# Performance work log

Measured on AMD Instinct MI355X. Metric: run time of the kernel, lower is better.

## Reference

```python
import jax, jax.numpy as jnp
import numpy as np
import math

H = 2048      # hidden_size
NH = 32       # num heads
HD = H // NH  # head_dim = 64
THETA = 10000.0
B, S = 2, 2048


def _rope_tables(seq_len):
    inv_freq = 1.0 / (THETA ** (jnp.arange(0, HD, 2, dtype=jnp.float32) / HD))
    t = jnp.arange(seq_len, dtype=jnp.float32)
    freqs = t[:, None] * inv_freq[None, :]          # [S, HD/2]
    emb = jnp.concatenate([freqs, freqs], axis=-1)  # [S, HD]
    return jnp.cos(emb)[None, None], jnp.sin(emb)[None, None]  # [1,1,S,HD]


def _rotate_half(x):
    x1, x2 = jnp.split(x, 2, axis=-1)
    return jnp.concatenate([-x2, x1], axis=-1)


def setup_inputs() -> dict:
    key = jax.random.key(0)
    ks = jax.random.split(key, 5)
    hidden_states = jax.random.normal(ks[0], (B, S, H), dtype=jnp.float32)
    wscale = 1.0 / math.sqrt(H)
    wq = jax.random.normal(ks[1], (H, H), dtype=jnp.float32) * wscale
    wk = jax.random.normal(ks[2], (H, H), dtype=jnp.float32) * wscale
    wv = jax.random.normal(ks[3], (H, H), dtype=jnp.float32) * wscale
    wo = jax.random.normal(ks[4], (H, H), dtype=jnp.float32) * wscale
    # additive causal mask: 0 on/below diagonal, -1e9 above
    causal = jnp.tril(jnp.ones((S, S), dtype=bool))
    attention_mask = jnp.where(causal, 0.0, -1e9).astype(jnp.float32)[None, None]
    return {"hidden_states": hidden_states, "attention_mask": attention_mask,
            "wq": wq, "wk": wk, "wv": wv, "wo": wo}


def reference(hidden_states, attention_mask, wq, wk, wv, wo):
    b, s, _ = hidden_states.shape
    # projections (Linear, no bias); weights stored [in, out]
    q = (hidden_states @ wq).reshape(b, s, NH, HD).transpose(0, 2, 1, 3)  # [B,NH,S,HD]
    k = (hidden_states @ wk).reshape(b, s, NH, HD).transpose(0, 2, 1, 3)
    v = (hidden_states @ wv).reshape(b, s, NH, HD).transpose(0, 2, 1, 3)
    # RoPE
    cos, sin = _rope_tables(s)
    q = q * cos + _rotate_half(q) * sin
    k = k * cos + _rotate_half(k) * sin
    # attention
    attn = jnp.einsum('bhqd,bhkd->bhqk', q, k) / math.sqrt(HD)
    attn = attn + attention_mask
    w = jax.nn.softmax(attn, axis=-1)
    out = jnp.einsum('bhqk,bhkd->bhqd', w, v)           # [B,NH,S,HD]
    out = out.transpose(0, 2, 1, 3).reshape(b, s, H)    # [B,S,H]
    return out @ wo
```

## Files before the change

kernel.cpp:

```cpp
#include <hip/hip_runtime.h>
#include <hip/hip_bf16.h>

#define H 2048
#define NH 32
#define HD 64
#define BB 2
#define SS 2048
#define MM (BB*SS)

typedef __attribute__((ext_vector_type(8))) short bf16x8;
typedef __attribute__((ext_vector_type(4))) float f32x4;
typedef __attribute__((ext_vector_type(16))) float f32x16;
typedef unsigned short u16;
typedef unsigned int u32;
typedef __attribute__((ext_vector_type(4))) u32 u32x4;

static __device__ __forceinline__ u16 f2bf(float f){
  union { float f; u32 i; } v; v.f = f;
  u32 x = v.i;
  return (u16)((x + 0x7FFFu + ((x >> 16) & 1u)) >> 16);
}
static __device__ __forceinline__ float bf2f(u16 u){
  union { u32 i; float f; } v; v.i = ((u32)u) << 16; return v.f;
}
static __device__ __forceinline__ u32 pk2(float a, float b){
  u32 r;
  asm("v_cvt_pk_bf16_f32 %0, %1, %2" : "=v"(r) : "v"(a), "v"(b));
  return r;
}

static __device__ __forceinline__ void gload16(const u16* g, u16* l){
  __builtin_amdgcn_global_load_lds((const __attribute__((address_space(1))) void*)g,
                                   (__attribute__((address_space(3))) void*)l, 16, 0, 0);
}

__global__ void k_cvt(const float* __restrict__ src, u16* __restrict__ dst){
  const int i = (blockIdx.x * 256 + threadIdx.x) * 4;
  float4 v = *(const float4*)(src + i);
  ushort4 o;
  o.x = f2bf(v.x); o.y = f2bf(v.y); o.z = f2bf(v.z); o.w = f2bf(v.w);
  *(ushort4*)(dst + i) = o;
}

__global__ void k_wtrans(const float* __restrict__ w0, const float* __restrict__ w1,
                         const float* __restrict__ w2, const float* __restrict__ w3,
                         u16* __restrict__ d0, u16* __restrict__ d1,
                         u16* __restrict__ d2, u16* __restrict__ d3){
  __shared__ float tile[32][33];
  const int z = blockIdx.z;
  const float* w = z==0 ? w0 : z==1 ? w1 : z==2 ? w2 : w3;
  u16* d        = z==0 ? d0 : z==1 ? d1 : z==2 ? d2 : d3;
  const int n0 = blockIdx.x * 32, k0 = blockIdx.y * 32;
  const int tx = threadIdx.x, ty = threadIdx.y;
  #pragma unroll
  for (int j = 0; j < 4; j++)
    tile[ty + 8*j][tx] = w[(size_t)(k0 + ty + 8*j) * H + n0 + tx];
  __syncthreads();
  #pragma unroll
  for (int j = 0; j < 4; j++)
    d[(size_t)(n0 + ty + 8*j) * H + k0 + tx] = f2bf(tile[tx][ty + 8*j]);
}

__global__ __launch_bounds__(512, 2) void k_gemm8(
    const u16* __restrict__ A, const u16* __restrict__ Bt,
    u16* __restrict__ CQ, u16* __restrict__ CK, u16* __restrict__ CV,
    int M, int K){
  __shared__ __align__(16) u16 As[2][128][64];
  __shared__ __align__(16) u16 Bs[2][384][64];
  const int flat = blockIdx.x;
  const int id = (flat & 7) * 64 + (flat >> 3);
  const int gy = id >> 5, gx = id & 31;
  const int m0 = gx * 128, n0 = gy * 384;
  const int t = threadIdx.x, w = t >> 6, l = t & 63;
  const int wm = w >> 2, wn = w & 3;
  const int lrow = l & 15, lk = (l >> 4) * 8;
  const int sw = (lrow & 7) * 8;
  const int sr = t >> 3, sc = (t & 7) * 8;
  const int ssc = sc ^ ((sr & 7) * 8);
  const int NK = K >> 6;

  auto stageA = [&](int kt, int u){
    const size_t kb = (size_t)kt * 64 + ssc;
    #pragma unroll
    for (int c = 0; c < 2; c++)
      gload16(A + (size_t)(m0 + c*64 + sr) * K + kb, &As[u][c*64 + sr][sc]);
  };
  auto stageB = [&](int kt, int u){
    const size_t kb = (size_t)kt * 64 + ssc;
    #pragma unroll
    for (int c = 0; c < 6; c++)
      gload16(Bt + (size_t)(n0 + c*64 + sr) * K + kb, &Bs[u][c*64 + sr][sc]);
  };

  f32x4 acc[4][6] = {};

  stageA(0, 0); stageB(0, 0);
  stageA(1, 1); stageB(1, 1);
  asm volatile("s_waitcnt vmcnt(8)" ::: "memory");
  __builtin_amdgcn_s_barrier();

  #pragma unroll 1
  for (int kt = 0; kt < NK; ++kt){
    const int u = kt & 1;
    const bool more = (kt + 2 < NK);
    bf16x8 b0[6], b1[6], a0, a1;

    #pragma unroll
    for (int n = 0; n < 6; n++)
      b0[n] = *(const bf16x8*)&Bs[u][wn*96 + n*16 + lrow][lk ^ sw];
    a0 = *(const bf16x8*)&As[u][wm*64 +  0 + lrow][lk ^ sw];
    a1 = *(const bf16x8*)&As[u][wm*64 + 16 + lrow][lk ^ sw];
    __builtin_amdgcn_s_setprio(1);
    #pragma unroll
    for (int n = 0; n < 6; n++){
      acc[0][n] = __builtin_amdgcn_mfma_f32_16x16x32_bf16(a0, b0[n], acc[0][n], 0, 0, 0);
      acc[1][n] = __builtin_amdgcn_mfma_f32_16x16x32_bf16(a1, b0[n], acc[1][n], 0, 0, 0);
    }
    __builtin_amdgcn_s_setprio(0);
    __builtin_amdgcn_s_barrier();

    #pragma unroll
    for (int n = 0; n < 6; n++)
      b1[n] = *(const bf16x8*)&Bs[u][wn*96 + n*16 + lrow][(32 + lk) ^ sw];
    a0 = *(const bf16x8*)&As[u][wm*64 +  0 + lrow][(32 + lk) ^ sw];
    a1 = *(const bf16x8*)&As[u][wm*64 + 16 + lrow][(32 + lk) ^ sw];
    __builtin_amdgcn_s_setprio(1);
    #pragma unroll
    for (int n = 0; n < 6; n++){
      acc[0][n] = __builtin_amdgcn_mfma_f32_16x16x32_bf16(a0, b1[n], acc[0][n], 0, 0, 0);
      acc[1][n] = __builtin_amdgcn_mfma_f32_16x16x32_bf16(a1, b1[n], acc[1][n], 0, 0, 0);
    }
    __builtin_amdgcn_s_setprio(0);
    __builtin_amdgcn_s_barrier();

    if (more) stageB(kt + 2, u);
    a0 = *(const bf16x8*)&As[u][wm*64 + 32 + lrow][lk ^ sw];
    a1 = *(const bf16x8*)&As[u][wm*64 + 48 + lrow][lk ^ sw];
    __builtin_amdgcn_s_setprio(1);
    #pragma unroll
    for (int n = 0; n < 6; n++){
      acc[2][n] = __builtin_amdgcn_mfma_f32_16x16x32_bf16(a0, b0[n], acc[2][n], 0, 0, 0);
      acc[3][n] = __builtin_amdgcn_mfma_f32_16x16x32_bf16(a1, b0[n], acc[3][n], 0, 0, 0);
    }
    __builtin_amdgcn_s_setprio(0);
    __builtin_amdgcn_s_barrier();

    a0 = *(const bf16x8*)&As[u][wm*64 + 32 + lrow][(32 + lk) ^ sw];
    a1 = *(const bf16x8*)&As[u][wm*64 + 48 + lrow][(32 + lk) ^ sw];
    __builtin_amdgcn_s_setprio(1);
    #pragma unroll
    for (int n = 0; n < 6; n++){
      acc[2][n] = __builtin_amdgcn_mfma_f32_16x16x32_bf16(a0, b1[n], acc[2][n], 0, 0, 0);
      acc[3][n] = __builtin_amdgcn_mfma_f32_16x16x32_bf16(a1, b1[n], acc[3][n], 0, 0, 0);
    }
    __builtin_amdgcn_s_setprio(0);
    __builtin_amdgcn_s_barrier();

    if (more){
      stageA(kt + 2, u);
      asm volatile("s_waitcnt vmcnt(8)" ::: "memory");
      __builtin_amdgcn_s_barrier();
    } else if (kt + 1 < NK){
      asm volatile("s_waitcnt vmcnt(0)" ::: "memory");
      __builtin_amdgcn_s_barrier();
    }
  }

  #pragma unroll
  for (int m = 0; m < 4; m++)
    #pragma unroll
    for (int n = 0; n < 6; n++){
      const int ncol = n0 + wn*96 + n*16 + lrow;
      const int z = ncol >> 11;
      u16* C = (z == 0 ? CQ : z == 1 ? CK : CV) + (ncol & 2047);
      #pragma unroll
      for (int r = 0; r < 4; r++){
        const int row = m0 + wm*64 + m*16 + (l >> 4)*4 + r;
        C[(size_t)row * H] = f2bf(acc[m][n][r]);
      }
    }
}

template<typename OutT>
__global__ __launch_bounds__(256, 2) void k_gemm(
    const u16* __restrict__ A,
    const u16* __restrict__ B0, const u16* __restrict__ B1, const u16* __restrict__ B2,
    OutT* __restrict__ C0, OutT* __restrict__ C1, OutT* __restrict__ C2,
    int M, int N, int K){
  __shared__ __align__(16) u16 As[128][64];
  __shared__ __align__(16) u16 Bs[128][64];
  const int z = blockIdx.z;
  const u16* Bt = z==0 ? B0 : z==1 ? B1 : B2;
  OutT* C       = z==0 ? C0 : z==1 ? C1 : C2;
  const int t = threadIdx.x;
  const int w = t >> 6, l = t & 63;
  const int m0 = blockIdx.x * 128, n0 = blockIdx.y * 128;
  const int srow = t >> 3, scol = (t & 7) * 8;
  const int lrow = l & 15, lk = (l >> 4) * 8;
  const int wr = (w >> 1) * 64, wc = (w & 1) * 64;
  f32x4 acc[4][4] = {};
  for (int k0 = 0; k0 < K; k0 += 64){
    __syncthreads();
    #pragma unroll
    for (int c = 0; c < 4; c++)
      gload16(A + (size_t)(m0 + c*32 + srow) * K + k0 + scol, &As[c*32 + srow][scol]);
    #pragma unroll
    for (int c = 0; c < 4; c++)
      gload16(Bt + (size_t)(n0 + c*32 + srow) * K + k0 + scol, &Bs[c*32 + srow][scol]);
    __syncthreads();
    #pragma unroll
    for (int kk = 0; kk < 2; kk++){
      bf16x8 a[4], b[4];
      #pragma unroll
      for (int m = 0; m < 4; m++) a[m] = *(const bf16x8*)&As[wr + m*16 + lrow][kk*32 + lk];
      #pragma unroll
      for (int n = 0; n < 4; n++) b[n] = *(const bf16x8*)&Bs[wc + n*16 + lrow][kk*32 + lk];
      #pragma unroll
      for (int m = 0; m < 4; m++)
        #pragma unroll
        for (int n = 0; n < 4; n++)
          acc[m][n] = __builtin_amdgcn_mfma_f32_16x16x32_bf16(a[m], b[n], acc[m][n], 0, 0, 0);
    }
  }
  #pragma unroll
  for (int m = 0; m < 4; m++)
    #pragma unroll
    for (int n = 0; n < 4; n++)
      #pragma unroll
      for (int r = 0; r < 4; r++){
        const int row = m0 + wr + m*16 + (l >> 4)*4 + r;
        const int col = n0 + wc + n*16 + lrow;
        const float v = acc[m][n][r];
        if constexpr (sizeof(OutT) == 2) C[(size_t)row * N + col] = (OutT)f2bf(v);
        else                             C[(size_t)row * N + col] = v;
      }
}

__global__ void k_rope(u16* __restrict__ Q, u16* __restrict__ Kp){
  const int idx = blockIdx.x * 256 + threadIdx.x;
  const int quad = idx & 3;
  const int h = (idx >> 2) & 31;
  const int row = idx >> 7;
  const int s = row & (SS - 1);
  const int i0 = quad * 8;
  u16* q = Q  + (size_t)row * H + h * HD;
  u16* k = Kp + (size_t)row * H + h * HD;
  uint4 q1v = *(const uint4*)(q + i0);
  uint4 q2v = *(const uint4*)(q + i0 + 32);
  uint4 k1v = *(const uint4*)(k + i0);
  uint4 k2v = *(const uint4*)(k + i0 + 32);
  u16* q1 = (u16*)&q1v; u16* q2 = (u16*)&q2v;
  u16* k1 = (u16*)&k1v; u16* k2 = (u16*)&k2v;
  const float sf = (float)s;
  const float QSC = 0.18033688011112042f;
  #pragma unroll
  for (int e = 0; e < 8; e++){
    const int i = i0 + e;
    const float inv = exp2f(-0.4152410118609203f * (float)i);
    float rev = sf * inv * 0.15915494309189535f;
    rev -= floorf(rev);
    const float sn = __builtin_amdgcn_sinf(rev);
    const float cs = __builtin_amdgcn_cosf(rev);
    const float qa = bf2f(q1[e]), qb = bf2f(q2[e]);
    q1[e] = f2bf((qa*cs - qb*sn) * QSC);
    q2[e] = f2bf((qb*cs + qa*sn) * QSC);
    const float ka = bf2f(k1[e]), kb = bf2f(k2[e]);
    k1[e] = f2bf(ka*cs - kb*sn);
    k2[e] = f2bf(kb*cs + ka*sn);
  }
  *(uint4*)(q + i0)      = q1v;
  *(uint4*)(q + i0 + 32) = q2v;
  *(uint4*)(k + i0)      = k1v;
  *(uint4*)(k + i0 + 32) = k2v;
}

__global__ __launch_bounds__(256, 2) void k_attn(
    const u16* __restrict__ Q, const u16* __restrict__ K,
    const u16* __restrict__ V, u16* __restrict__ O){
  __shared__ __align__(16) u16 Ks[3][64][64];
  __shared__ __align__(16) u16 Vs[2][64][72];
  const int t = threadIdx.x, w = t >> 6, l = t & 63;
  const int x = blockIdx.x, bh = blockIdx.y;
  const int b = bh >> 5, h = bh & 31;
  const u16* kp = K + (size_t)(b*SS) * H + h * HD;
  const u16* vp = V + (size_t)(b*SS) * H + h * HD;
  const int sr = t >> 3, sc = (t & 7) * 8;
  const int ssc = sc ^ ((sr & 7) * 8);
  const int hi = l >> 5, lq = l & 31;

  auto stageK = [&](int tile, int buf){
    const int jb = tile * 64;
    gload16(kp + (size_t)(jb + sr) * H + ssc,      &Ks[buf][sr][sc]);
    gload16(kp + (size_t)(jb + 32 + sr) * H + ssc, &Ks[buf][32 + sr][sc]);
  };
  auto loadV = [&](int tile, uint4* vv){
    const int jb = tile * 64;
    vv[0] = *(const uint4*)(vp + (size_t)(jb + sr) * H + sc);
    vv[1] = *(const uint4*)(vp + (size_t)(jb + 32 + sr) * H + sc);
  };
  auto publishV = [&](const uint4* vv, int buf){
    #pragma unroll
    for (int c = 0; c < 2; c++){
      const int j = c*32 + sr;
      const u16* pv = (const u16*)&vv[c];
      #pragma unroll
      for (int e = 0; e < 8; e++){
        const int d = sc + e;
        Vs[buf][d][j ^ ((d >> 3) * 8)] = pv[e];
      }
    }
  };

  #pragma unroll 1
  for (int pp = 0; pp < 2; pp++){
    const int qt = pp ? x : (15 - x);
    const int NT = 2*qt + 2;
    const int qw0 = qt*128 + w*32;
    const int qrow = qw0 + lq;

    const u16* qptr = Q + (size_t)(b*SS + qrow) * H + h * HD + hi*8;
    bf16x8 qf[4];
    #pragma unroll
    for (int c = 0; c < 4; c++) qf[c] = *(const bf16x8*)(qptr + c*16);

    float mrun = -1e30f, lrun = 0.f;
    f32x16 oacc[2] = {};
    uint4 vvE[2], vvO[2];

    stageK(0, 0); loadV(0, vvE);
    stageK(1, 1); loadV(1, vvO);
    asm volatile("s_waitcnt vmcnt(4)" ::: "memory");
    publishV(vvE, 0);
    asm volatile("s_waitcnt lgkmcnt(0)" ::: "memory");
    __builtin_amdgcn_s_barrier();

    auto body = [&](int jt, int p, uint4* vvSelf, const uint4* vvOther){
      const int j0 = jt * 64;
      if (jt + 2 < NT){ stageK(jt + 2, (jt + 2) % 3); loadV(jt + 2, vvSelf); }

      if (j0 <= qw0){
        const int kbuf = jt % 3;
        f32x16 sv[2] = {};
        __builtin_amdgcn_s_setprio(1);
        #pragma unroll
        for (int kb = 0; kb < 2; kb++){
          const int row = kb*32 + lq;
          #pragma unroll
          for (int c = 0; c < 4; c++){
            bf16x8 kf = *(const bf16x8*)&Ks[kbuf][row][(c*16 + hi*8) ^ ((row & 7) * 8)];
            sv[kb] = __builtin_amdgcn_mfma_f32_32x32x16_bf16(kf, qf[c], sv[kb], 0, 0, 0);
          }
        }
        __builtin_amdgcn_s_setprio(0);
        if (j0 + 63 > qw0){
          #pragma unroll
          for (int kb = 0; kb < 2; kb++)
            #pragma unroll
            for (int r = 0; r < 16; r++){
              const int kg = j0 + kb*32 + (r & 3) + 8*(r >> 2) + 4*hi;
              if (kg > qrow) sv[kb][r] = -1e30f;
            }
        }
        float t16[16], t8[8], t4[4];
        #pragma unroll
        for (int r = 0; r < 16; r++) t16[r] = fmaxf(sv[0][r], sv[1][r]);
        #pragma unroll
        for (int r = 0; r < 8; r++) t8[r] = fmaxf(t16[r], t16[r+8]);
        #pragma unroll
        for (int r = 0; r < 4; r++) t4[r] = fmaxf(t8[r], t8[r+4]);
        float tm = fmaxf(fmaxf(t4[0], t4[2]), fmaxf(t4[1], t4[3]));
        tm = fmaxf(tm, __shfl_xor(tm, 32, 64));
        if (__any(tm > mrun)){
          const float mn = fmaxf(mrun, tm);
          const float fac = exp2f(mrun - mn);
          mrun = mn;
          lrun *= fac;
          #pragma unroll
          for (int db = 0; db < 2; db++)
            #pragma unroll
            for (int r = 0; r < 16; r++) oacc[db][r] *= fac;
        }
        #pragma unroll
        for (int kb = 0; kb < 2; kb++)
          #pragma unroll
          for (int r = 0; r < 16; r++) sv[kb][r] = exp2f(sv[kb][r] - mrun);
        float s16[16], s8[8], s4[4];
        #pragma unroll
        for (int r = 0; r < 16; r++) s16[r] = sv[0][r] + sv[1][r];
        #pragma unroll
        for (int r = 0; r < 8; r++) s8[r] = s16[r] + s16[r+8];
        #pragma unroll
        for (int r = 0; r < 4; r++) s4[r] = s8[r] + s8[r+4];
        float rs = (s4[0] + s4[1]) + (s4[2] + s4[3]);
        rs += __shfl_xor(rs, 32, 64);
        lrun += rs;
        u32x4 pw[4];
        #pragma unroll
        for (int kb = 0; kb < 2; kb++){
          #pragma unroll
          for (int half = 0; half < 2; half++){
            const int rb = half * 8;
            const u32 own0 = pk2(sv[kb][rb+0], sv[kb][rb+1]);
            const u32 own1 = pk2(sv[kb][rb+2], sv[kb][rb+3]);
            const u32 own2 = pk2(sv[kb][rb+4], sv[kb][rb+5]);
            const u32 own3 = pk2(sv[kb][rb+6], sv[kb][rb+7]);
            const u32 s0 = hi ? own0 : own2;
            const u32 s1 = hi ? own1 : own3;
            const u32 r0 = __shfl_xor(s0, 32, 64);
            const u32 r1 = __shfl_xor(s1, 32, 64);
            u32x4 pv;
            pv[0] = hi ? r0 : own0;
            pv[1] = hi ? r1 : own1;
            pv[2] = hi ? own2 : r0;
            pv[3] = hi ? own3 : r1;
            pw[kb*2 + half] = pv;
          }
        }
        __builtin_amdgcn_s_setprio(1);
        #pragma unroll
        for (int db = 0; db < 2; db++){
          const int d = db*32 + lq;
          #pragma unroll
          for (int tt = 0; tt < 4; tt++){
            bf16x8 vf = *(const bf16x8*)&Vs[p][d][(tt*16 + hi*8) ^ ((d >> 3) * 8)];
            bf16x8 pfr = __builtin_bit_cast(bf16x8, pw[tt]);
            oacc[db] = __builtin_amdgcn_mfma_f32_32x32x16_bf16(vf, pfr, oacc[db], 0, 0, 0);
          }
        }
        __builtin_amdgcn_s_setprio(0);
      }

      if (jt + 2 < NT) asm volatile("s_waitcnt vmcnt(4)" ::: "memory");
      else             asm volatile("s_waitcnt vmcnt(0)" ::: "memory");
      if (jt + 1 < NT) publishV(vvOther, p ^ 1);
      asm volatile("s_waitcnt lgkmcnt(0)" ::: "memory");
      __builtin_amdgcn_s_barrier();
    };

    #pragma unroll 1
    for (int jt2 = 0; jt2 < NT; jt2 += 2){
      body(jt2,     0, vvE, vvO);
      body(jt2 + 1, 1, vvO, vvE);
    }

    const float rl = 1.0f / lrun;
    u16* op = O + (size_t)(b*SS + qrow) * H + h * HD;
    #pragma unroll
    for (int db = 0; db < 2; db++)
      #pragma unroll
      for (int rq = 0; rq < 4; rq++){
        ushort4 o4;
        o4.x = f2bf(oacc[db][rq*4 + 0] * rl);
        o4.y = f2bf(oacc[db][rq*4 + 1] * rl);
        o4.z = f2bf(oacc[db][rq*4 + 2] * rl);
        o4.w = f2bf(oacc[db][rq*4 + 3] * rl);
        *(ushort4*)(op + db*32 + rq*8 + 4*hi) = o4;
      }
  }
}

extern "C" void kernel_launch(void* const* d_in, const int* in_sizes, int n_in,
                              void* d_out, int out_size, void* d_ws, size_t ws_size,
                              hipStream_t stream){
  (void)in_sizes; (void)n_in; (void)out_size; (void)ws_size;
  const float* hs = (const float*)d_in[0];
  const float* wq = (const float*)d_in[2];
  const float* wk = (const float*)d_in[3];
  const float* wv = (const float*)d_in[4];
  const float* wo = (const float*)d_in[5];
  float* out = (float*)d_out;
  char* ws = (char*)d_ws;

  u16* Xb  = (u16*)ws;
  u16* Wqt = (u16*)(ws + (size_t)MM * H * 2);
  u16* Wkt = Wqt + (size_t)H * H;
  u16* Wvt = Wkt + (size_t)H * H;
  u16* Wot = Wvt + (size_t)H * H;
  u16* Vb  = Wot + (size_t)H * H;
  u16* Ob  = Vb  + (size_t)MM * H;
  u16* Qb  = (u16*)d_out;
  u16* Kb  = Qb + (size_t)MM * H;

  k_cvt<<<8192, 256, 0, stream>>>(hs, Xb);
  k_wtrans<<<dim3(64, 64, 4), dim3(32, 8), 0, stream>>>(wq, wk, wv, wo, Wqt, Wkt, Wvt, Wot);
  k_gemm8<<<512, 512, 0, stream>>>(Xb, Wqt, Qb, Kb, Vb, MM, H);
  k_rope<<<2048, 256, 0, stream>>>(Qb, Kb);
  k_attn<<<dim3(8, 64), 256, 0, stream>>>(Qb, Kb, Vb, Ob);
  k_gemm<float><<<dim3(32, 16, 1), 256, 0, stream>>>(Ob, Wot, Wot, Wot, out, out, out, MM, H, H);
}
```

Before: 296.0 us.

## Restructure QKV GEMM inner loop into four phases with explicit LDS wait scheduling

After: 319.1 us. +7.8%, slower.

```diff
diff --git a/kernel.cpp b/kernel.cpp
--- a/kernel.cpp
+++ b/kernel.cpp
@@ -103,61 +103,77 @@
   for (int kt = 0; kt < NK; ++kt){
     const int u = kt & 1;
     const bool more = (kt + 2 < NK);
-    bf16x8 b0[6], b1[6], a0, a1;
-
-    #pragma unroll
-    for (int n = 0; n < 6; n++)
-      b0[n] = *(const bf16x8*)&Bs[u][wn*96 + n*16 + lrow][lk ^ sw];
-    a0 = *(const bf16x8*)&As[u][wm*64 +  0 + lrow][lk ^ sw];
-    a1 = *(const bf16x8*)&As[u][wm*64 + 16 + lrow][lk ^ sw];
+    bf16x8 a[4], b[3];
+
+    #pragma unroll
+    for (int mb = 0; mb < 4; mb++)
+      a[mb] = *(const bf16x8*)&As[u][wm*64 + mb*16 + lrow][lk ^ sw];
+    #pragma unroll
+    for (int nb = 0; nb < 3; nb++)
+      b[nb] = *(const bf16x8*)&Bs[u][wn*96 + nb*16 + lrow][lk ^ sw];
+    __builtin_amdgcn_sched_barrier(0);
+    __builtin_amdgcn_s_barrier();
+    asm volatile("s_waitcnt lgkmcnt(0)" ::: "memory");
     __builtin_amdgcn_s_setprio(1);
     #pragma unroll
-    for (int n = 0; n < 6; n++){
-      acc[0][n] = __builtin_amdgcn_mfma_f32_16x16x32_bf16(a0, b0[n], acc[0][n], 0, 0, 0);
-      acc[1][n] = __builtin_amdgcn_mfma_f32_16x16x32_bf16(a1, b0[n], acc[1][n], 0, 0, 0);
-    }
+    for (int mb = 0; mb < 4; mb++)
+      #pragma unroll
+      for (int nb = 0; nb < 3; nb++)
+        acc[mb][nb] = __builtin_amdgcn_mfma_f32_16x16x32_bf16(a[mb], b[nb], acc[mb][nb], 0, 0, 0);
     __builtin_amdgcn_s_setprio(0);
     __builtin_amdgcn_s_barrier();
 
     #pragma unroll
-    for (int n = 0; n < 6; n++)
-      b1[n] = *(const bf16x8*)&Bs[u][wn*96 + n*16 + lrow][(32 + lk) ^ sw];
-    a0 = *(const bf16x8*)&As[u][wm*64 +  0 + lrow][(32 + lk) ^ sw];
-    a1 = *(const bf16x8*)&As[u][wm*64 + 16 + lrow][(32 + lk) ^ sw];
+    for (int nb = 0; nb < 3; nb++)
+      b[nb] = *(const bf16x8*)&Bs[u][wn*96 + 48 + nb*16 + lrow][lk ^ sw];
+    __builtin_amdgcn_sched_barrier(0);
+    __builtin_amdgcn_s_barrier();
+    asm volatile("s_waitcnt lgkmcnt(0)" ::: "memory");
     __builtin_amdgcn_s_setprio(1);
     #pragma unroll
-    for (int n = 0; n < 6; n++){
-      acc[0][n] = __builtin_amdgcn_mfma_f32_16x16x32_bf16(a0, b1[n], acc[0][n], 0, 0, 0);
-      acc[1][n] = __builtin_amdgcn_mfma_f32_16x16x32_bf16(a1, b1[n], acc[1][n], 0, 0, 0);
-    }
+    for (int mb = 0; mb < 4; mb++)
+      #pragma unroll
+      for (int nb = 0; nb < 3; nb++)
+        acc[mb][3 + nb] = __builtin_amdgcn_mfma_f32_16x16x32_bf16(a[mb], b[nb], acc[mb][3 + nb], 0, 0, 0);
     __builtin_amdgcn_s_setprio(0);
     __builtin_amdgcn_s_barrier();
 
-    if (more) stageB(kt + 2, u);
-    a0 = *(const bf16x8*)&As[u][wm*64 + 32 + lrow][lk ^ sw];
-    a1 = *(const bf16x8*)&As[u][wm*64 + 48 + lrow][lk ^ sw];
+    #pragma unroll
+    for (int mb = 0; mb < 4; mb++)
+      a[mb] = *(const bf16x8*)&As[u][wm*64 + mb*16 + lrow][(32 + lk) ^ sw];
+    #pragma unroll
+    for (int nb = 0; nb < 3; nb++)
+      b[nb] = *(const bf16x8*)&Bs[u][wn*96 + nb*16 + lrow][(32 + lk) ^ sw];
+    __builtin_amdgcn_sched_barrier(0);
+    __builtin_amdgcn_s_barrier();
+    asm volatile("s_waitcnt lgkmcnt(0)" ::: "memory");
     __builtin_amdgcn_s_setprio(1);
     #pragma unroll
-    for (int n = 0; n < 6; n++){
-      acc[2][n] = __builtin_amdgcn_mfma_f32_16x16x32_bf16(a0, b0[n], acc[2][n], 0, 0, 0);
-      acc[3][n] = __builtin_amdgcn_mfma_f32_16x16x32_bf16(a1, b0[n], acc[3][n], 0, 0, 0);
-    }
+    for (int mb = 0; mb < 4; mb++)
+      #pragma unroll
+      for (int nb = 0; nb < 3; nb++)
+        acc[mb][nb] = __builtin_amdgcn_mfma_f32_16x16x32_bf16(a[mb], b[nb], acc[mb][nb], 0, 0, 0);
     __builtin_amdgcn_s_setprio(0);
     __builtin_amdgcn_s_barrier();
 
-    a0 = *(const bf16x8*)&As[u][wm*64 + 32 + lrow][(32 + lk) ^ sw];
-    a1 = *(const bf16x8*)&As[u][wm*64 + 48 + lrow][(32 + lk) ^ sw];
+    #pragma unroll
+    for (int nb = 0; nb < 3; nb++)
+      b[nb] = *(const bf16x8*)&Bs[u][wn*96 + 48 + nb*16 + lrow][(32 + lk) ^ sw];
+    if (more) stageA(kt + 2, u);
+    __builtin_amdgcn_sched_barrier(0);
+    __builtin_amdgcn_s_barrier();
+    asm volatile("s_waitcnt lgkmcnt(0)" ::: "memory");
     __builtin_amdgcn_s_setprio(1);
     #pragma unroll
-    for (int n = 0; n < 6; n++){
-      acc[2][n] = __builtin_amdgcn_mfma_f32_16x16x32_bf16(a0, b1[n], acc[2][n], 0, 0, 0);
-      acc[3][n] = __builtin_amdgcn_mfma_f32_16x16x32_bf16(a1, b1[n], acc[3][n], 0, 0, 0);
-    }
+    for (int mb = 0; mb < 4; mb++)
+      #pragma unroll
+      for (int nb = 0; nb < 3; nb++)
+        acc[mb][3 + nb] = __builtin_amdgcn_mfma_f32_16x16x32_bf16(a[mb], b[nb], acc[mb][3 + nb], 0, 0, 0);
     __builtin_amdgcn_s_setprio(0);
     __builtin_amdgcn_s_barrier();
 
     if (more){
-      stageA(kt + 2, u);
+      stageB(kt + 2, u);
       asm volatile("s_waitcnt vmcnt(8)" ::: "memory");
       __builtin_amdgcn_s_barrier();
     } else if (kt + 1 < NK){
```

## Pipeline output projection GEMM with double-buffered LDS and fuse Q RoPE into attention

Applied to the files above, without the earlier changes.

After: 287.8 us. 2.8% less time.

```diff
diff --git a/kernel.cpp b/kernel.cpp
--- a/kernel.cpp
+++ b/kernel.cpp
@@ -181,78 +181,135 @@
     }
 }
 
-template<typename OutT>
-__global__ __launch_bounds__(256, 2) void k_gemm(
-    const u16* __restrict__ A,
-    const u16* __restrict__ B0, const u16* __restrict__ B1, const u16* __restrict__ B2,
-    OutT* __restrict__ C0, OutT* __restrict__ C1, OutT* __restrict__ C2,
-    int M, int N, int K){
-  __shared__ __align__(16) u16 As[128][64];
-  __shared__ __align__(16) u16 Bs[128][64];
-  const int z = blockIdx.z;
-  const u16* Bt = z==0 ? B0 : z==1 ? B1 : B2;
-  OutT* C       = z==0 ? C0 : z==1 ? C1 : C2;
-  const int t = threadIdx.x;
-  const int w = t >> 6, l = t & 63;
-  const int m0 = blockIdx.x * 128, n0 = blockIdx.y * 128;
-  const int srow = t >> 3, scol = (t & 7) * 8;
+__global__ __launch_bounds__(512, 2) void k_gemmo(
+    const u16* __restrict__ A, const u16* __restrict__ Bt,
+    float* __restrict__ C, int M, int N, int K){
+  __shared__ __align__(16) u16 As[2][128][64];
+  __shared__ __align__(16) u16 Bs[2][256][64];
+  const int flat = blockIdx.x;
+  const int id = (flat & 7) * 32 + (flat >> 3);
+  const int gy = id >> 5, gx = id & 31;
+  const int m0 = gx * 128, n0 = gy * 256;
+  const int t = threadIdx.x, w = t >> 6, l = t & 63;
+  const int wm = w >> 2, wn = w & 3;
   const int lrow = l & 15, lk = (l >> 4) * 8;
-  const int wr = (w >> 1) * 64, wc = (w & 1) * 64;
+  const int sw = (lrow & 7) * 8;
+  const int sr = t >> 3, sc = (t & 7) * 8;
+  const int ssc = sc ^ ((sr & 7) * 8);
+  const int NK = K >> 6;
+
+  auto stageA = [&](int kt, int u){
+    const size_t kb = (size_t)kt * 64 + ssc;
+    #pragma unroll
+    for (int c = 0; c < 2; c++)
+      gload16(A + (size_t)(m0 + c*64 + sr) * K + kb, &As[u][c*64 + sr][sc]);
+  };
+  auto stageB = [&](int kt, int u){
+    const size_t kb = (size_t)kt * 64 + ssc;
+    #pragma unroll
+    for (int c = 0; c < 4; c++)
+      gload16(Bt + (size_t)(n0 + c*64 + sr) * K + kb, &Bs[u][c*64 + sr][sc]);
+  };
+
   f32x4 acc[4][4] = {};
-  for (int k0 = 0; k0 < K; k0 += 64){
-    __syncthreads();
-    #pragma unroll
-    for (int c = 0; c < 4; c++)
-      gload16(A + (size_t)(m0 + c*32 + srow) * K + k0 + scol, &As[c*32 + srow][scol]);
-    #pragma unroll
-    for (int c = 0; c < 4; c++)
-      gload16(Bt + (size_t)(n0 + c*32 + srow) * K + k0 + scol, &Bs[c*32 + srow][scol]);
-    __syncthreads();
-    #pragma unroll
-    for (int kk = 0; kk < 2; kk++){
-      bf16x8 a[4], b[4];
-      #pragma unroll
-      for (int m = 0; m < 4; m++) a[m] = *(const bf16x8*)&As[wr + m*16 + lrow][kk*32 + lk];
-      #pragma unroll
-      for (int n = 0; n < 4; n++) b[n] = *(const bf16x8*)&Bs[wc + n*16 + lrow][kk*32 + lk];
-      #pragma unroll
-      for (int m = 0; m < 4; m++)
-        #pragma unroll
-        for (int n = 0; n < 4; n++)
-          acc[m][n] = __builtin_amdgcn_mfma_f32_16x16x32_bf16(a[m], b[n], acc[m][n], 0, 0, 0);
+
+  stageA(0, 0); stageB(0, 0);
+  stageA(1, 1); stageB(1, 1);
+  asm volatile("s_waitcnt vmcnt(6)" ::: "memory");
+  __builtin_amdgcn_s_barrier();
+
+  #pragma unroll 1
+  for (int kt = 0; kt < NK; ++kt){
+    const int u = kt & 1;
+    const bool more = (kt + 2 < NK);
+    bf16x8 b0[4], b1[4], a0, a1;
+
+    #pragma unroll
+    for (int n = 0; n < 4; n++)
+      b0[n] = *(const bf16x8*)&Bs[u][wn*64 + n*16 + lrow][lk ^ sw];
+    a0 = *(const bf16x8*)&As[u][wm*64 +  0 + lrow][lk ^ sw];
+    a1 = *(const bf16x8*)&As[u][wm*64 + 16 + lrow][lk ^ sw];
+    __builtin_amdgcn_s_setprio(1);
+    #pragma unroll
+    for (int n = 0; n < 4; n++){
+      acc[0][n] = __builtin_amdgcn_mfma_f32_16x16x32_bf16(a0, b0[n], acc[0][n], 0, 0, 0);
+      acc[1][n] = __builtin_amdgcn_mfma_f32_16x16x32_bf16(a1, b0[n], acc[1][n], 0, 0, 0);
+    }
+    __builtin_amdgcn_s_setprio(0);
+    __builtin_amdgcn_s_barrier();
+
+    #pragma unroll
+    for (int n = 0; n < 4; n++)
+      b1[n] = *(const bf16x8*)&Bs[u][wn*64 + n*16 + lrow][(32 + lk) ^ sw];
+    a0 = *(const bf16x8*)&As[u][wm*64 +  0 + lrow][(32 + lk) ^ sw];
+    a1 = *(const bf16x8*)&As[u][wm*64 + 16 + lrow][(32 + lk) ^ sw];
+    __builtin_amdgcn_s_setprio(1);
+    #pragma unroll
+    for (int n = 0; n < 4; n++){
+      acc[0][n] = __builtin_amdgcn_mfma_f32_16x16x32_bf16(a0, b1[n], acc[0][n], 0, 0, 0);
+      acc[1][n] = __builtin_amdgcn_mfma_f32_16x16x32_bf16(a1, b1[n], acc[1][n], 0, 0, 0);
+    }
+    __builtin_amdgcn_s_setprio(0);
+    __builtin_amdgcn_s_barrier();
+
+    if (more) stageB(kt + 2, u);
+    a0 = *(const bf16x8*)&As[u][wm*64 + 32 + lrow][lk ^ sw];
+    a1 = *(const bf16x8*)&As[u][wm*64 + 48 + lrow][lk ^ sw];
+    __builtin_amdgcn_s_setprio(1);
+    #pragma unroll
+    for (int n = 0; n < 4; n++){
+      acc[2][n] = __builtin_amdgcn_mfma_f32_16x16x32_bf16(a0, b0[n], acc[2][n], 0, 0, 0);
+      acc[3][n] = __builtin_amdgcn_mfma_f32_16x16x32_bf16(a1, b0[n], acc[3][n], 0, 0, 0);
+    }
+    __builtin_amdgcn_s_setprio(0);
+    __builtin_amdgcn_s_barrier();
+
+    a0 = *(const bf16x8*)&As[u][wm*64 + 32 + lrow][(32 + lk) ^ sw];
+    a1 = *(const bf16x8*)&As[u][wm*64 + 48 + lrow][(32 + lk) ^ sw];
+    __builtin_amdgcn_s_setprio(1);
+    #pragma unroll
+    for (int n = 0; n < 4; n++){
+      acc[2][n] = __builtin_amdgcn_mfma_f32_16x16x32_bf16(a0, b1[n], acc[2][n], 0, 0, 0);
+      acc[3][n] = __builtin_amdgcn_mfma_f32_16x16x32_bf16(a1, b1[n], acc[3][n], 0, 0, 0);
+    }
+    __builtin_amdgcn_s_setprio(0);
+    __builtin_amdgcn_s_barrier();
+
+    if (more){
+      stageA(kt + 2, u);
+      asm volatile("s_waitcnt vmcnt(6)" ::: "memory");
+      __builtin_amdgcn_s_barrier();
+    } else if (kt + 1 < NK){
+      asm volatile("s_waitcnt vmcnt(0)" ::: "memory");
+      __builtin_amdgcn_s_barrier();
     }
   }
+
   #pragma unroll
   for (int m = 0; m < 4; m++)
     #pragma unroll
-    for (int n = 0; n < 4; n++)
+    for (int n = 0; n < 4; n++){
+      const int col = n0 + wn*64 + n*16 + lrow;
       #pragma unroll
       for (int r = 0; r < 4; r++){
-        const int row = m0 + wr + m*16 + (l >> 4)*4 + r;
-        const int col = n0 + wc + n*16 + lrow;
-        const float v = acc[m][n][r];
-        if constexpr (sizeof(OutT) == 2) C[(size_t)row * N + col] = (OutT)f2bf(v);
-        else                             C[(size_t)row * N + col] = v;
+        const int row = m0 + wm*64 + m*16 + (l >> 4)*4 + r;
+        C[(size_t)row * N + col] = acc[m][n][r];
       }
-}
-
-__global__ void k_rope(u16* __restrict__ Q, u16* __restrict__ Kp){
+    }
+}
+
+__global__ void k_rope(u16* __restrict__ Kp){
   const int idx = blockIdx.x * 256 + threadIdx.x;
   const int quad = idx & 3;
   const int h = (idx >> 2) & 31;
   const int row = idx >> 7;
   const int s = row & (SS - 1);
   const int i0 = quad * 8;
-  u16* q = Q  + (size_t)row * H + h * HD;
   u16* k = Kp + (size_t)row * H + h * HD;
-  uint4 q1v = *(const uint4*)(q + i0);
-  uint4 q2v = *(const uint4*)(q + i0 + 32);
   uint4 k1v = *(const uint4*)(k + i0);
   uint4 k2v = *(const uint4*)(k + i0 + 32);
-  u16* q1 = (u16*)&q1v; u16* q2 = (u16*)&q2v;
   u16* k1 = (u16*)&k1v; u16* k2 = (u16*)&k2v;
   const float sf = (float)s;
-  const float QSC = 0.18033688011112042f;
   #pragma unroll
   for (int e = 0; e < 8; e++){
     const int i = i0 + e;
@@ -261,15 +318,10 @@
     rev -= floorf(rev);
     const float sn = __builtin_amdgcn_sinf(rev);
     const float cs = __builtin_amdgcn_cosf(rev);
-    const float qa = bf2f(q1[e]), qb = bf2f(q2[e]);
-    q1[e] = f2bf((qa*cs - qb*sn) * QSC);
-    q2[e] = f2bf((qb*cs + qa*sn) * QSC);
     const float ka = bf2f(k1[e]), kb = bf2f(k2[e]);
     k1[e] = f2bf(ka*cs - kb*sn);
     k2[e] = f2bf(kb*cs + ka*sn);
   }
-  *(uint4*)(q + i0)      = q1v;
-  *(uint4*)(q + i0 + 32) = q2v;
   *(uint4*)(k + i0)      = k1v;
   *(uint4*)(k + i0 + 32) = k2v;
 }
@@ -287,6 +339,7 @@
   const int sr = t >> 3, sc = (t & 7) * 8;
   const int ssc = sc ^ ((sr & 7) * 8);
   const int hi = l >> 5, lq = l & 31;
+  const float QSC = 0.18033688011112042f;
 
   auto stageK = [&](int tile, int buf){
     const int jb = tile * 64;
@@ -319,9 +372,32 @@
     const int qrow = qw0 + lq;
 
     const u16* qptr = Q + (size_t)(b*SS + qrow) * H + h * HD + hi*8;
+    bf16x8 qr0 = *(const bf16x8*)(qptr + 0);
+    bf16x8 qr1 = *(const bf16x8*)(qptr + 16);
+    bf16x8 qr2 = *(const bf16x8*)(qptr + 32);
+    bf16x8 qr3 = *(const bf16x8*)(qptr + 48);
     bf16x8 qf[4];
-    #pragma unroll
-    for (int c = 0; c < 4; c++) qf[c] = *(const bf16x8*)(qptr + c*16);
+    {
+      const float sf = (float)qrow;
+      #pragma unroll
+      for (int e = 0; e < 8; e++){
+        #pragma unroll
+        for (int pr = 0; pr < 2; pr++){
+          const int d = pr*16 + hi*8 + e;
+          const float inv = exp2f(-0.4152410118609203f * (float)d);
+          float rev = sf * inv * 0.15915494309189535f;
+          rev -= floorf(rev);
+          const float sn = __builtin_amdgcn_sinf(rev);
+          const float cs = __builtin_amdgcn_cosf(rev);
+          const float qa = bf2f((u16)(pr ? qr1[e] : qr0[e]));
+          const float qb = bf2f((u16)(pr ? qr3[e] : qr2[e]));
+          const u16 oa = f2bf((qa*cs - qb*sn) * QSC);
+          const u16 ob = f2bf((qb*cs + qa*sn) * QSC);
+          if (pr){ qf[1][e] = (short)oa; qf[3][e] = (short)ob; }
+          else   { qf[0][e] = (short)oa; qf[2][e] = (short)ob; }
+        }
+      }
+    }
 
     float mrun = -1e30f, lrun = 0.f;
     f32x16 oacc[2] = {};
@@ -484,7 +560,7 @@
   k_cvt<<<8192, 256, 0, stream>>>(hs, Xb);
   k_wtrans<<<dim3(64, 64, 4), dim3(32, 8), 0, stream>>>(wq, wk, wv, wo, Wqt, Wkt, Wvt, Wot);
   k_gemm8<<<512, 512, 0, stream>>>(Xb, Wqt, Qb, Kb, Vb, MM, H);
-  k_rope<<<2048, 256, 0, stream>>>(Qb, Kb);
+  k_rope<<<2048, 256, 0, stream>>>(Kb);
   k_attn<<<dim3(8, 64), 256, 0, stream>>>(Qb, Kb, Vb, Ob);
-  k_gemm<float><<<dim3(32, 16, 1), 256, 0, stream>>>(Ob, Wot, Wot, Wot, out, out, out, MM, H, H);
-}
+  k_gemmo<<<256, 512, 0, stream>>>(Ob, Wot, out, MM, H, H);
+}
```
